# Performance work log

Measured on AMD Instinct MI355X. Metric: run time of the kernel, lower is better.

The kernel has to match this reference:

```python
import jax, jax.numpy as jnp
import numpy as np


def setup_inputs() -> dict:
    key = jax.random.key(0)
    ks = jax.random.split(key, 16)
    B, S, H, E, C = 256, 512, 1024, 512, 10

    def kaiming(k, d1, d2):
        # kaiming_normal_ with nonlinearity='linear': std = 1/sqrt(fan_in)=1/sqrt(d2)
        return jax.random.normal(k, (d1, d2), dtype=jnp.float32) / jnp.sqrt(jnp.float32(d2))

    return {
        "x": jax.random.randint(ks[0], (B, S), 0, 3, dtype=jnp.int64),
        "emb": jax.random.normal(ks[1], (3, E), dtype=jnp.float32),
        "w_cx": kaiming(ks[2], E, H), "b_c": jnp.zeros((H,), jnp.float32),
        "w_ix": kaiming(ks[3], E, H), "w_ih": kaiming(ks[4], H, H), "b_i": jnp.zeros((H,), jnp.float32),
        "w_fx": kaiming(ks[5], E, H), "w_fh": kaiming(ks[6], H, H), "b_f": jnp.zeros((H,), jnp.float32),
        "w_ox": kaiming(ks[7], E, H), "w_oh": kaiming(ks[8], H, H), "b_o": jnp.zeros((H,), jnp.float32),
        "w_ph": kaiming(ks[9], H, C), "b_p": jnp.zeros((C,), jnp.float32),
    }


def _peep_lstm(x, emb, w_cx, b_c, w_ix, w_ih, b_i, w_fx, w_fh, b_f,
               w_ox, w_oh, b_o, w_ph, b_p):
    B, S = x.shape
    H = w_ih.shape[0]
    ex = emb[x]                                   # [B, S, E]
    pad = ((x + 1) // 2).astype(emb.dtype)        # [B, S], in {0,1}
    # Precompute input-to-gate projections for steps 0..S-2 (same math as per-step matmul)
    exs = ex[:, :S - 1, :]                        # [B, S-1, E]
    gi = jnp.einsum('bse,eh->sbh', exs, w_ix) + b_i
    gf = jnp.einsum('bse,eh->sbh', exs, w_fx) + b_f
    go = jnp.einsum('bse,eh->sbh', exs, w_ox) + b_o
    gc = jnp.einsum('bse,eh->sbh', exs, w_cx) + b_c
    pads = pad[:, :S - 1].T                       # [S-1, B]

    def step(carry, inp):
        c, _h = carry
        xi, xf, xo, xc, p = inp
        i = jax.nn.sigmoid(xi + c @ w_ih)
        f = jax.nn.sigmoid(xf + c @ w_fh)
        o = jax.nn.sigmoid(xo + c @ w_oh)
        c = jax.nn.sigmoid(xc) * i + c * f
        h = jnp.tanh(c) * o * p[:, None]
        return (c, h), None

    c0 = jnp.zeros((B, H), dtype=emb.dtype)
    h0 = jnp.zeros((B, H), dtype=emb.dtype)
    (c_fin, h_fin), _ = jax.lax.scan(step, (c0, h0), (gi, gf, go, gc, pads))
    p_out = h_fin @ w_ph + b_p
    # Faithful to the original: log_softmax over dim=0 (the batch dim)
    return jax.nn.log_softmax(p_out, axis=0)


def reference(x, emb, w_cx, b_c, w_ix, w_ih, b_i, w_fx, w_fh, b_f,
              w_ox, w_oh, b_o, w_ph, b_p):
    return _peep_lstm(x, emb, w_cx, b_c, w_ix, w_ih, b_i, w_fx, w_fh, b_f,
                      w_ox, w_oh, b_o, w_ph, b_p)
```

## Files before the change

### kernel.cpp

```cpp
#include <hip/hip_runtime.h>
#include <hip/hip_bf16.h>
#include <hip/hip_fp16.h>

typedef __attribute__((ext_vector_type(8))) _Float16 f16x8;
typedef __attribute__((ext_vector_type(4))) float f32x4;

#define NSTEP 511

__device__ __forceinline__ unsigned short f2h(float f){ return __half_as_ushort(__float2half(f)); }
__device__ __forceinline__ float sigf(float z){ return 1.0f/(1.0f + __expf(-z)); }

__device__ __forceinline__ void st32_coh(unsigned* p, unsigned v){
  asm volatile("global_store_dword %0, %1, off sc0 sc1\n\ts_waitcnt vmcnt(0)"
               :: "v"(p), "v"(v) : "memory");
}
__device__ __forceinline__ unsigned ld32_coh(const unsigned* p){
  unsigned v;
  asm volatile("global_load_dword %0, %1, off sc0 sc1\n\ts_waitcnt vmcnt(0)"
               : "=v"(v) : "v"(p) : "memory");
  return v;
}
__device__ __forceinline__ void ldA8_coh(const void* p, f16x8 a[8]){
  asm volatile(
    "global_load_dwordx4 %0, %8, off sc0 sc1\n\t"
    "global_load_dwordx4 %1, %8, off offset:64 sc0 sc1\n\t"
    "global_load_dwordx4 %2, %8, off offset:128 sc0 sc1\n\t"
    "global_load_dwordx4 %3, %8, off offset:192 sc0 sc1\n\t"
    "global_load_dwordx4 %4, %8, off offset:256 sc0 sc1\n\t"
    "global_load_dwordx4 %5, %8, off offset:320 sc0 sc1\n\t"
    "global_load_dwordx4 %6, %8, off offset:384 sc0 sc1\n\t"
    "global_load_dwordx4 %7, %8, off offset:448 sc0 sc1\n\t"
    "s_waitcnt vmcnt(0)"
    : "=v"(a[0]),"=v"(a[1]),"=v"(a[2]),"=v"(a[3]),
      "=v"(a[4]),"=v"(a[5]),"=v"(a[6]),"=v"(a[7])
    : "v"(p) : "memory");
}

__global__ void k_tables(const float* __restrict__ emb, const float* __restrict__ w,
                         const float* __restrict__ bias, float* __restrict__ T){
  int h = blockIdx.x*256 + threadIdx.x;
  float a0=0.f, a1=0.f, a2=0.f;
  for(int e=0;e<512;e++){
    float we = w[e*1024 + h];
    a0 += emb[e]*we; a1 += emb[512+e]*we; a2 += emb[1024+e]*we;
  }
  float b = bias[h];
  T[h] = a0+b; T[1024+h] = a1+b; T[2048+h] = a2+b;
}

__global__ void k_transpose(const float* __restrict__ w, unsigned short* __restrict__ wT){
  __shared__ float tile[64][65];
  int tr = blockIdx.x & 15, tc = blockIdx.x >> 4;
  int col = threadIdx.x & 63;
  int r0  = threadIdx.x >> 6;
  for(int rr=0; rr<16; rr++){
    int row = rr*4 + r0;
    tile[row][col] = w[(tr*64+row)*1024 + tc*64 + col];
  }
  __syncthreads();
  for(int rr=0; rr<16; rr++){
    int row = rr*4 + r0;
    wT[(tc*64+row)*1024 + tr*64 + col] = f2h(tile[col][row]);
  }
}

__global__ void __launch_bounds__(512,1) k_recur(
    const int* __restrict__ x,
    const unsigned short* __restrict__ wTi,
    const unsigned short* __restrict__ wTf,
    const unsigned short* __restrict__ wTo,
    const float* __restrict__ Ti, const float* __restrict__ Tf,
    const float* __restrict__ To, const float* __restrict__ Tc,
    unsigned short* __restrict__ cbf,
    float* __restrict__ hbuf,
    unsigned int* __restrict__ bars)
{
  __shared__ __align__(16) float xch[8192];
  __shared__ __align__(16) float xo[4096];

  const int tid  = threadIdx.x;
  const int wid  = tid >> 6;
  const int lane = tid & 63;
  const int mg   = blockIdx.x & 7;
  const int ng   = blockIdx.x >> 3;
  const int mbase = mg*32;
  const int nbase = ng*32;

  const int mh_w = wid & 1;
  const int q_w  = wid >> 1;

  const int bcol0 = nbase + (lane&15);
  const int bcol1 = nbase + 16 + (lane&15);
  const int bk    = q_w*256 + (lane>>4)*8;
  f16x8 Bi0[8], Bi1[8], Bf0[8], Bf1[8];
  #pragma unroll
  for(int kk=0;kk<8;kk++){
    Bi0[kk] = *reinterpret_cast<const f16x8*>(wTi + bcol0*1024 + bk + kk*32);
    Bi1[kk] = *reinterpret_cast<const f16x8*>(wTi + bcol1*1024 + bk + kk*32);
    Bf0[kk] = *reinterpret_cast<const f16x8*>(wTf + bcol0*1024 + bk + kk*32);
    Bf1[kk] = *reinterpret_cast<const f16x8*>(wTf + bcol1*1024 + bk + kk*32);
  }

  const int b_l = tid >> 4;
  const int h_l = (tid & 15)*2;
  const int bg  = mbase + b_l;

  float tT[3][3][2];
  { const float* Tp[3] = {Ti, Tf, Tc};
    #pragma unroll
    for(int g=0; g<3; g++)
      #pragma unroll
      for(int v=0; v<3; v++)
        #pragma unroll
        for(int j=0; j<2; j++) tT[g][v][j] = Tp[g][v*1024 + nbase + h_l + j];
  }
  float cm0 = 0.f, cm1 = 0.f;

  const int arow = mh_w*16 + (lane&15);
  const int aoff = q_w*256 + (lane>>4)*8;
  unsigned int* arr = bars + mg*64;

  int vc = x[bg*512];

  for(int t=0; t<NSTEP; t++){
    const bool last = (t == NSTEP-1);
    const unsigned short* rdp = cbf + (unsigned)(t&1)*262144u;
    unsigned short*       wrp = cbf + (unsigned)((t+1)&1)*262144u;

    if(t > 0){
      const unsigned tgt = (unsigned)t;
      const unsigned* slot = arr + q_w*8 + (lane&7);
      while(true){
        unsigned v = ld32_coh(slot);
        if(__all((int)(v >= tgt))) break;
        __builtin_amdgcn_s_sleep(1);
      }
    }

    f16x8 ah[8];
    ldA8_coh(rdp + (mbase + arow)*1024 + aoff, ah);
    int vn = last ? 0 : x[bg*512 + t + 1];

    f32x4 a00={0.f,0.f,0.f,0.f}, a01={0.f,0.f,0.f,0.f};
    f32x4 a10={0.f,0.f,0.f,0.f}, a11={0.f,0.f,0.f,0.f};
    #pragma unroll
    for(int kk=0;kk<8;kk++){
      a00 = __builtin_amdgcn_mfma_f32_16x16x32_f16(ah[kk], Bi0[kk], a00, 0,0,0);
      a01 = __builtin_amdgcn_mfma_f32_16x16x32_f16(ah[kk], Bi1[kk], a01, 0,0,0);
      a10 = __builtin_amdgcn_mfma_f32_16x16x32_f16(ah[kk], Bf0[kk], a10, 0,0,0);
      a11 = __builtin_amdgcn_mfma_f32_16x16x32_f16(ah[kk], Bf1[kk], a11, 0,0,0);
    }
    *reinterpret_cast<f32x4*>(xch + (wid*4 + 0)*256 + lane*4) = a00;
    *reinterpret_cast<f32x4*>(xch + (wid*4 + 1)*256 + lane*4) = a01;
    *reinterpret_cast<f32x4*>(xch + (wid*4 + 2)*256 + lane*4) = a10;
    *reinterpret_cast<f32x4*>(xch + (wid*4 + 3)*256 + lane*4) = a11;
    if(last){
      f32x4 o0={0.f,0.f,0.f,0.f}, o1={0.f,0.f,0.f,0.f};
      #pragma unroll
      for(int kk=0;kk<8;kk++){
        f16x8 bo0 = *reinterpret_cast<const f16x8*>(wTo + bcol0*1024 + bk + kk*32);
        f16x8 bo1 = *reinterpret_cast<const f16x8*>(wTo + bcol1*1024 + bk + kk*32);
        o0 = __builtin_amdgcn_mfma_f32_16x16x32_f16(ah[kk], bo0, o0, 0,0,0);
        o1 = __builtin_amdgcn_mfma_f32_16x16x32_f16(ah[kk], bo1, o1, 0,0,0);
      }
      *reinterpret_cast<f32x4*>(xo + (wid*2 + 0)*256 + lane*4) = o0;
      *reinterpret_cast<f32x4*>(xo + (wid*2 + 1)*256 + lane*4) = o1;
    }
    __syncthreads();

    {
      const int v = vc;
      int r16 = b_l & 15;
      int mh  = b_l >> 4;
      int reg = r16 & 3;
      int lq  = r16 >> 2;
      float cn[2], hh[2];
      #pragma unroll
      for(int j=0;j<2;j++){
        int col = h_l + j;
        int nh  = col >> 4;
        int l   = (lq<<4) | (col & 15);
        float mi = 0.f, mf = 0.f;
        #pragma unroll
        for(int q=0;q<4;q++){
          const float* base = xch + ((q*2+mh)*4 + nh)*256 + l*4 + reg;
          mi += base[0];
          mf += base[512];
        }
        float ti = (v==0)?tT[0][0][j]:(v==1)?tT[0][1][j]:tT[0][2][j];
        float tf = (v==0)?tT[1][0][j]:(v==1)?tT[1][1][j]:tT[1][2][j];
        float tc = (v==0)?tT[2][0][j]:(v==1)?tT[2][1][j]:tT[2][2][j];
        float iv = sigf(ti + mi);
        float fv = sigf(tf + mf);
        float cv = sigf(tc);
        float cm = j ? cm1 : cm0;
        float c2 = cv*iv + cm*fv;
        cn[j] = c2;
        if(last){
          float mo = 0.f;
          #pragma unroll
          for(int q=0;q<4;q++) mo += xo[((q*2+mh)*2 + nh)*256 + l*4 + reg];
          float to = To[v*1024 + nbase + col];
          float ov = sigf(to + mo);
          float pad = (float)((v+1)>>1);
          hh[j] = tanhf(c2)*ov*pad;
        }
      }
      if(!last){
        cm0 = cn[0]; cm1 = cn[1];
        unsigned pk = (unsigned)f2h(cn[0]) | (((unsigned)f2h(cn[1]))<<16);
        st32_coh(reinterpret_cast<unsigned*>(wrp + bg*1024 + nbase + h_l), pk);
      } else {
        *reinterpret_cast<float2*>(hbuf + bg*1024 + nbase + h_l) = make_float2(hh[0], hh[1]);
      }
    }

    if(!last){
      __syncthreads();
      if(tid == 0) st32_coh(&arr[ng], (unsigned)(t+1));
    }
    vc = vn;
  }
}

__global__ void k_proj(const float* __restrict__ hbuf, const float* __restrict__ w_ph,
                       const float* __restrict__ b_p, float* __restrict__ out){
  const int c = blockIdx.x;
  const int b = threadIdx.x;
  float acc = b_p[c];
  const float4* hb = reinterpret_cast<const float4*>(hbuf + b*1024);
  for(int i=0;i<256;i++){
    float4 hv = hb[i];
    int h = i*4;
    acc += hv.x*w_ph[h*10+c] + hv.y*w_ph[(h+1)*10+c] + hv.z*w_ph[(h+2)*10+c] + hv.w*w_ph[(h+3)*10+c];
  }
  __shared__ float red[256];
  red[b] = acc; __syncthreads();
  for(int s=128;s>0;s>>=1){ if(b<s) red[b]=fmaxf(red[b],red[b+s]); __syncthreads(); }
  float m = red[0]; __syncthreads();
  red[b] = expf(acc-m); __syncthreads();
  for(int s=128;s>0;s>>=1){ if(b<s) red[b]+=red[b+s]; __syncthreads(); }
  out[b*10+c] = acc - m - logf(red[0]);
}

extern "C" void kernel_launch(void* const* d_in, const int* in_sizes, int n_in,
                              void* d_out, int out_size, void* d_ws, size_t ws_size,
                              hipStream_t stream){
  const int*   x    = (const int*)  d_in[0];
  const float* emb  = (const float*)d_in[1];
  const float* w_cx = (const float*)d_in[2];
  const float* b_c  = (const float*)d_in[3];
  const float* w_ix = (const float*)d_in[4];
  const float* w_ih = (const float*)d_in[5];
  const float* b_i  = (const float*)d_in[6];
  const float* w_fx = (const float*)d_in[7];
  const float* w_fh = (const float*)d_in[8];
  const float* b_f  = (const float*)d_in[9];
  const float* w_ox = (const float*)d_in[10];
  const float* w_oh = (const float*)d_in[11];
  const float* b_o  = (const float*)d_in[12];
  const float* w_ph = (const float*)d_in[13];
  const float* b_p  = (const float*)d_in[14];
  float* out = (float*)d_out;

  char* ws = (char*)d_ws;
  float* Ti = (float*)(ws);
  float* Tf = (float*)(ws + 12288);
  float* To = (float*)(ws + 24576);
  float* Tc = (float*)(ws + 36864);
  unsigned short* wTi = (unsigned short*)(ws + 49152);
  unsigned short* wTf = (unsigned short*)(ws + 2146304);
  unsigned short* wTo = (unsigned short*)(ws + 4243456);
  unsigned short* cbf = (unsigned short*)(ws + 6340608);
  unsigned int*  bars = (unsigned int*) (ws + 7389184);
  float* hbuf = (float*)(ws + 7391232);

  hipMemsetAsync(cbf, 0, 1048576 + 2048, stream);
  k_tables<<<4,256,0,stream>>>(emb, w_ix, b_i, Ti);
  k_tables<<<4,256,0,stream>>>(emb, w_fx, b_f, Tf);
  k_tables<<<4,256,0,stream>>>(emb, w_ox, b_o, To);
  k_tables<<<4,256,0,stream>>>(emb, w_cx, b_c, Tc);
  k_transpose<<<256,256,0,stream>>>(w_ih, wTi);
  k_transpose<<<256,256,0,stream>>>(w_fh, wTf);
  k_transpose<<<256,256,0,stream>>>(w_oh, wTo);

  void* args[] = { (void*)&x, (void*)&wTi, (void*)&wTf, (void*)&wTo,
                   (void*)&Ti, (void*)&Tf, (void*)&To, (void*)&Tc,
                   (void*)&cbf, (void*)&hbuf, (void*)&bars };
  hipLaunchCooperativeKernel((void*)k_recur, dim3(256), dim3(512), args, 0, stream);
  k_proj<<<10,256,0,stream>>>(hbuf, w_ph, b_p, out);
}
```

Before: 2.499 ms.

## Replace barrier counters with step-tagged cell values for flag-free synchronization

Each fp16 cell value is now stored in a 32-bit word whose upper half carries the step number. Consumers spin directly on loading their A operand until every tag matches the expected step, which removes the per-block __syncthreads, the flag store and the separate flag polling. The cost is twice the bytes per exchange, a larger double buffer, repacking with perm, and reloading all 16 vectors on every spin iteration. It also relies on the 64-bit store becoming visible as a unit, and on the step tag fitting in 16 bits.

```diff
diff --git a/kernel.cpp b/kernel.cpp
--- a/kernel.cpp
+++ b/kernel.cpp
@@ -4,35 +4,40 @@
 
 typedef __attribute__((ext_vector_type(8))) _Float16 f16x8;
 typedef __attribute__((ext_vector_type(4))) float f32x4;
+typedef __attribute__((ext_vector_type(4))) unsigned int u32x4;
 
 #define NSTEP 511
 
 __device__ __forceinline__ unsigned short f2h(float f){ return __half_as_ushort(__float2half(f)); }
 __device__ __forceinline__ float sigf(float z){ return 1.0f/(1.0f + __expf(-z)); }
 
-__device__ __forceinline__ void st32_coh(unsigned* p, unsigned v){
-  asm volatile("global_store_dword %0, %1, off sc0 sc1\n\ts_waitcnt vmcnt(0)"
-               :: "v"(p), "v"(v) : "memory");
-}
-__device__ __forceinline__ unsigned ld32_coh(const unsigned* p){
-  unsigned v;
-  asm volatile("global_load_dword %0, %1, off sc0 sc1\n\ts_waitcnt vmcnt(0)"
-               : "=v"(v) : "v"(p) : "memory");
-  return v;
-}
-__device__ __forceinline__ void ldA8_coh(const void* p, f16x8 a[8]){
+__device__ __forceinline__ void st64_coh(unsigned* p, unsigned lo, unsigned hi){
+  unsigned long long v = ((unsigned long long)hi << 32) | (unsigned long long)lo;
+  asm volatile("global_store_dwordx2 %0, %1, off sc0 sc1" :: "v"(p), "v"(v) : "memory");
+}
+__device__ __forceinline__ void ldA16_coh(const unsigned* p, u32x4 r[16]){
   asm volatile(
-    "global_load_dwordx4 %0, %8, off sc0 sc1\n\t"
-    "global_load_dwordx4 %1, %8, off offset:64 sc0 sc1\n\t"
-    "global_load_dwordx4 %2, %8, off offset:128 sc0 sc1\n\t"
-    "global_load_dwordx4 %3, %8, off offset:192 sc0 sc1\n\t"
-    "global_load_dwordx4 %4, %8, off offset:256 sc0 sc1\n\t"
-    "global_load_dwordx4 %5, %8, off offset:320 sc0 sc1\n\t"
-    "global_load_dwordx4 %6, %8, off offset:384 sc0 sc1\n\t"
-    "global_load_dwordx4 %7, %8, off offset:448 sc0 sc1\n\t"
+    "global_load_dwordx4 %0, %16, off sc0 sc1\n\t"
+    "global_load_dwordx4 %1, %16, off offset:16 sc0 sc1\n\t"
+    "global_load_dwordx4 %2, %16, off offset:128 sc0 sc1\n\t"
+    "global_load_dwordx4 %3, %16, off offset:144 sc0 sc1\n\t"
+    "global_load_dwordx4 %4, %16, off offset:256 sc0 sc1\n\t"
+    "global_load_dwordx4 %5, %16, off offset:272 sc0 sc1\n\t"
+    "global_load_dwordx4 %6, %16, off offset:384 sc0 sc1\n\t"
+    "global_load_dwordx4 %7, %16, off offset:400 sc0 sc1\n\t"
+    "global_load_dwordx4 %8, %16, off offset:512 sc0 sc1\n\t"
+    "global_load_dwordx4 %9, %16, off offset:528 sc0 sc1\n\t"
+    "global_load_dwordx4 %10, %16, off offset:640 sc0 sc1\n\t"
+    "global_load_dwordx4 %11, %16, off offset:656 sc0 sc1\n\t"
+    "global_load_dwordx4 %12, %16, off offset:768 sc0 sc1\n\t"
+    "global_load_dwordx4 %13, %16, off offset:784 sc0 sc1\n\t"
+    "global_load_dwordx4 %14, %16, off offset:896 sc0 sc1\n\t"
+    "global_load_dwordx4 %15, %16, off offset:912 sc0 sc1\n\t"
     "s_waitcnt vmcnt(0)"
-    : "=v"(a[0]),"=v"(a[1]),"=v"(a[2]),"=v"(a[3]),
-      "=v"(a[4]),"=v"(a[5]),"=v"(a[6]),"=v"(a[7])
+    : "=v"(r[0]),"=v"(r[1]),"=v"(r[2]),"=v"(r[3]),
+      "=v"(r[4]),"=v"(r[5]),"=v"(r[6]),"=v"(r[7]),
+      "=v"(r[8]),"=v"(r[9]),"=v"(r[10]),"=v"(r[11]),
+      "=v"(r[12]),"=v"(r[13]),"=v"(r[14]),"=v"(r[15])
     : "v"(p) : "memory");
 }
 
@@ -71,9 +76,8 @@
     const unsigned short* __restrict__ wTo,
     const float* __restrict__ Ti, const float* __restrict__ Tf,
     const float* __restrict__ To, const float* __restrict__ Tc,
-    unsigned short* __restrict__ cbf,
-    float* __restrict__ hbuf,
-    unsigned int* __restrict__ bars)
+    unsigned* __restrict__ cpl,
+    float* __restrict__ hbuf)
 {
   __shared__ __align__(16) float xch[8192];
   __shared__ __align__(16) float xo[4096];
@@ -90,7 +94,7 @@
   const int q_w  = wid >> 1;
 
   const int bcol0 = nbase + (lane&15);
-  const int bcol1 = nbase + 16 + (lane&15);
+  const int bcol1 = bcol0 + 16;
   const int bk    = q_w*256 + (lane>>4)*8;
   f16x8 Bi0[8], Bi1[8], Bf0[8], Bf1[8];
   #pragma unroll
@@ -117,29 +121,41 @@
   float cm0 = 0.f, cm1 = 0.f;
 
   const int arow = mh_w*16 + (lane&15);
-  const int aoff = q_w*256 + (lane>>4)*8;
-  unsigned int* arr = bars + mg*64;
+  const int aoff = q_w*256 + ((lane>>4)<<3);
 
   int vc = x[bg*512];
 
   for(int t=0; t<NSTEP; t++){
     const bool last = (t == NSTEP-1);
-    const unsigned short* rdp = cbf + (unsigned)(t&1)*262144u;
-    unsigned short*       wrp = cbf + (unsigned)((t+1)&1)*262144u;
-
-    if(t > 0){
-      const unsigned tgt = (unsigned)t;
-      const unsigned* slot = arr + q_w*8 + (lane&7);
-      while(true){
-        unsigned v = ld32_coh(slot);
-        if(__all((int)(v >= tgt))) break;
-        __builtin_amdgcn_s_sleep(1);
+    const unsigned* rdp = cpl + (unsigned)(t&1)*262144u;
+    unsigned*       wrp = cpl + (unsigned)((t+1)&1)*262144u;
+    const unsigned texp = ((unsigned)t) << 16;
+
+    u32x4 r[16];
+    const unsigned* ap = rdp + (mbase+arow)*1024 + aoff;
+    while(true){
+      ldA16_coh(ap, r);
+      unsigned acc = 0u;
+      #pragma unroll
+      for(int i=0;i<16;i++){
+        acc |= (r[i][0]^texp); acc |= (r[i][1]^texp);
+        acc |= (r[i][2]^texp); acc |= (r[i][3]^texp);
       }
-    }
+      if(__all((int)((acc & 0xFFFF0000u) == 0u))) break;
+      __builtin_amdgcn_s_sleep(1);
+    }
+    int vn = last ? 0 : x[bg*512 + t + 1];
 
     f16x8 ah[8];
-    ldA8_coh(rdp + (mbase + arow)*1024 + aoff, ah);
-    int vn = last ? 0 : x[bg*512 + t + 1];
+    #pragma unroll
+    for(int kk=0;kk<8;kk++){
+      union { unsigned u[4]; f16x8 v; } uu;
+      uu.u[0] = __builtin_amdgcn_perm(r[2*kk][1],   r[2*kk][0],   0x05040100u);
+      uu.u[1] = __builtin_amdgcn_perm(r[2*kk][3],   r[2*kk][2],   0x05040100u);
+      uu.u[2] = __builtin_amdgcn_perm(r[2*kk+1][1], r[2*kk+1][0], 0x05040100u);
+      uu.u[3] = __builtin_amdgcn_perm(r[2*kk+1][3], r[2*kk+1][2], 0x05040100u);
+      ah[kk] = uu.v;
+    }
 
     f32x4 a00={0.f,0.f,0.f,0.f}, a01={0.f,0.f,0.f,0.f};
     f32x4 a10={0.f,0.f,0.f,0.f}, a11={0.f,0.f,0.f,0.f};
@@ -208,16 +224,13 @@
       }
       if(!last){
         cm0 = cn[0]; cm1 = cn[1];
-        unsigned pk = (unsigned)f2h(cn[0]) | (((unsigned)f2h(cn[1]))<<16);
-        st32_coh(reinterpret_cast<unsigned*>(wrp + bg*1024 + nbase + h_l), pk);
+        unsigned tp = ((unsigned)(t+1)) << 16;
+        unsigned p0 = tp | (unsigned)f2h(cn[0]);
+        unsigned p1 = tp | (unsigned)f2h(cn[1]);
+        st64_coh(wrp + bg*1024 + nbase + h_l, p0, p1);
       } else {
         *reinterpret_cast<float2*>(hbuf + bg*1024 + nbase + h_l) = make_float2(hh[0], hh[1]);
       }
-    }
-
-    if(!last){
-      __syncthreads();
-      if(tid == 0) st32_coh(&arr[ng], (unsigned)(t+1));
     }
     vc = vn;
   }
@@ -271,11 +284,10 @@
   unsigned short* wTi = (unsigned short*)(ws + 49152);
   unsigned short* wTf = (unsigned short*)(ws + 2146304);
   unsigned short* wTo = (unsigned short*)(ws + 4243456);
-  unsigned short* cbf = (unsigned short*)(ws + 6340608);
-  unsigned int*  bars = (unsigned int*) (ws + 7389184);
-  float* hbuf = (float*)(ws + 7391232);
-
-  hipMemsetAsync(cbf, 0, 1048576 + 2048, stream);
+  unsigned* cpl = (unsigned*)(ws + 6340608);
+  float* hbuf = (float*)(ws + 8437760);
+
+  hipMemsetAsync(cpl, 0, 2097152, stream);
   k_tables<<<4,256,0,stream>>>(emb, w_ix, b_i, Ti);
   k_tables<<<4,256,0,stream>>>(emb, w_fx, b_f, Tf);
   k_tables<<<4,256,0,stream>>>(emb, w_ox, b_o, To);
@@ -286,7 +298,7 @@
 
   void* args[] = { (void*)&x, (void*)&wTi, (void*)&wTf, (void*)&wTo,
                    (void*)&Ti, (void*)&Tf, (void*)&To, (void*)&Tc,
-                   (void*)&cbf, (void*)&hbuf, (void*)&bars };
-  hipLaunchCooperativeKernel((void*)k_recur, dim3(256), dim3(512), args, 0, stream);
+                   (void*)&cpl, (void*)&hbuf };
+  (void)hipLaunchCooperativeKernel((void*)k_recur, dim3(256), dim3(512), args, 0, stream);
   k_proj<<<10,256,0,stream>>>(hbuf, w_ph, b_p, out);
 }
```

After: 6.321 ms. 2.53x slower.

## Replace per-block step barrier with per-wave flags and double-buffered LDS

Applied to the files above, without the earlier changes.

Each wave now publishes its own progress flag after waiting only on its own stores, instead of the block running a second __syncthreads and thread 0 writing one flag per block. Consumer waves spin on the 64 wave flags covering the hidden-state slice they read, with no s_sleep between polls. The LDS exchange buffer is double-buffered by step parity so the removed barrier does not cause write-after-read hazards. The aim is a shorter critical path per recurrent step, at the cost of more flag traffic, tighter spinning and twice the LDS exchange footprint.

```diff
diff --git a/kernel.cpp b/kernel.cpp
--- a/kernel.cpp
+++ b/kernel.cpp
@@ -10,9 +10,8 @@
 __device__ __forceinline__ unsigned short f2h(float f){ return __half_as_ushort(__float2half(f)); }
 __device__ __forceinline__ float sigf(float z){ return 1.0f/(1.0f + __expf(-z)); }
 
-__device__ __forceinline__ void st32_coh(unsigned* p, unsigned v){
-  asm volatile("global_store_dword %0, %1, off sc0 sc1\n\ts_waitcnt vmcnt(0)"
-               :: "v"(p), "v"(v) : "memory");
+__device__ __forceinline__ void st32_coh_nw(unsigned* p, unsigned v){
+  asm volatile("global_store_dword %0, %1, off sc0 sc1" :: "v"(p), "v"(v) : "memory");
 }
 __device__ __forceinline__ unsigned ld32_coh(const unsigned* p){
   unsigned v;
@@ -73,9 +72,9 @@
     const float* __restrict__ To, const float* __restrict__ Tc,
     unsigned short* __restrict__ cbf,
     float* __restrict__ hbuf,
-    unsigned int* __restrict__ bars)
+    unsigned* __restrict__ bars)
 {
-  __shared__ __align__(16) float xch[8192];
+  __shared__ __align__(16) float xch[16384];
   __shared__ __align__(16) float xo[4096];
 
   const int tid  = threadIdx.x;
@@ -90,7 +89,7 @@
   const int q_w  = wid >> 1;
 
   const int bcol0 = nbase + (lane&15);
-  const int bcol1 = nbase + 16 + (lane&15);
+  const int bcol1 = bcol0 + 16;
   const int bk    = q_w*256 + (lane>>4)*8;
   f16x8 Bi0[8], Bi1[8], Bf0[8], Bf1[8];
   #pragma unroll
@@ -117,8 +116,9 @@
   float cm0 = 0.f, cm1 = 0.f;
 
   const int arow = mh_w*16 + (lane&15);
-  const int aoff = q_w*256 + (lane>>4)*8;
-  unsigned int* arr = bars + mg*64;
+  const int aoff = q_w*256 + ((lane>>4)<<3);
+  const unsigned* pollp = bars + (mg*256 + q_w*64 + lane);
+  unsigned* flagp = bars + (mg*256 + ng*8 + wid);
 
   int vc = x[bg*512];
 
@@ -129,11 +129,9 @@
 
     if(t > 0){
       const unsigned tgt = (unsigned)t;
-      const unsigned* slot = arr + q_w*8 + (lane&7);
       while(true){
-        unsigned v = ld32_coh(slot);
+        unsigned v = ld32_coh(pollp);
         if(__all((int)(v >= tgt))) break;
-        __builtin_amdgcn_s_sleep(1);
       }
     }
 
@@ -150,10 +148,11 @@
       a10 = __builtin_amdgcn_mfma_f32_16x16x32_f16(ah[kk], Bf0[kk], a10, 0,0,0);
       a11 = __builtin_amdgcn_mfma_f32_16x16x32_f16(ah[kk], Bf1[kk], a11, 0,0,0);
     }
-    *reinterpret_cast<f32x4*>(xch + (wid*4 + 0)*256 + lane*4) = a00;
-    *reinterpret_cast<f32x4*>(xch + (wid*4 + 1)*256 + lane*4) = a01;
-    *reinterpret_cast<f32x4*>(xch + (wid*4 + 2)*256 + lane*4) = a10;
-    *reinterpret_cast<f32x4*>(xch + (wid*4 + 3)*256 + lane*4) = a11;
+    float* xb = xch + (unsigned)(t&1)*8192u;
+    *reinterpret_cast<f32x4*>(xb + (wid*4 + 0)*256 + lane*4) = a00;
+    *reinterpret_cast<f32x4*>(xb + (wid*4 + 1)*256 + lane*4) = a01;
+    *reinterpret_cast<f32x4*>(xb + (wid*4 + 2)*256 + lane*4) = a10;
+    *reinterpret_cast<f32x4*>(xb + (wid*4 + 3)*256 + lane*4) = a11;
     if(last){
       f32x4 o0={0.f,0.f,0.f,0.f}, o1={0.f,0.f,0.f,0.f};
       #pragma unroll
@@ -183,7 +182,7 @@
         float mi = 0.f, mf = 0.f;
         #pragma unroll
         for(int q=0;q<4;q++){
-          const float* base = xch + ((q*2+mh)*4 + nh)*256 + l*4 + reg;
+          const float* base = xb + ((q*2+mh)*4 + nh)*256 + l*4 + reg;
           mi += base[0];
           mf += base[512];
         }
@@ -209,15 +208,15 @@
       if(!last){
         cm0 = cn[0]; cm1 = cn[1];
         unsigned pk = (unsigned)f2h(cn[0]) | (((unsigned)f2h(cn[1]))<<16);
-        st32_coh(reinterpret_cast<unsigned*>(wrp + bg*1024 + nbase + h_l), pk);
+        st32_coh_nw(reinterpret_cast<unsigned*>(wrp + bg*1024 + nbase + h_l), pk);
       } else {
         *reinterpret_cast<float2*>(hbuf + bg*1024 + nbase + h_l) = make_float2(hh[0], hh[1]);
       }
     }
 
     if(!last){
-      __syncthreads();
-      if(tid == 0) st32_coh(&arr[ng], (unsigned)(t+1));
+      asm volatile("s_waitcnt vmcnt(0)" ::: "memory");
+      if(lane == 0) st32_coh_nw(flagp, (unsigned)(t+1));
     }
     vc = vn;
   }
@@ -272,10 +271,10 @@
   unsigned short* wTf = (unsigned short*)(ws + 2146304);
   unsigned short* wTo = (unsigned short*)(ws + 4243456);
   unsigned short* cbf = (unsigned short*)(ws + 6340608);
-  unsigned int*  bars = (unsigned int*) (ws + 7389184);
-  float* hbuf = (float*)(ws + 7391232);
-
-  hipMemsetAsync(cbf, 0, 1048576 + 2048, stream);
+  unsigned* bars = (unsigned*)(ws + 7389184);
+  float* hbuf = (float*)(ws + 7397376);
+
+  hipMemsetAsync(cbf, 0, 1048576 + 8192, stream);
   k_tables<<<4,256,0,stream>>>(emb, w_ix, b_i, Ti);
   k_tables<<<4,256,0,stream>>>(emb, w_fx, b_f, Tf);
   k_tables<<<4,256,0,stream>>>(emb, w_ox, b_o, To);
@@ -287,6 +286,6 @@
   void* args[] = { (void*)&x, (void*)&wTi, (void*)&wTf, (void*)&wTo,
                    (void*)&Ti, (void*)&Tf, (void*)&To, (void*)&Tc,
                    (void*)&cbf, (void*)&hbuf, (void*)&bars };
-  hipLaunchCooperativeKernel((void*)k_recur, dim3(256), dim3(512), args, 0, stream);
+  (void)hipLaunchCooperativeKernel((void*)k_recur, dim3(256), dim3(512), args, 0, stream);
   k_proj<<<10,256,0,stream>>>(hbuf, w_ph, b_p, out);
 }
```

After: 5.176 ms. 107% more time.
